# Optimization experiments

Hardware: AMD Instinct MI355X
Metric: run time of the kernel (lower is better)

The kernel has to match this reference:

```python
import jax, jax.numpy as jnp
import numpy as np

N_QUBITS = 12
LAYERS = 8
N_CLASS = 10
BATCH = 2048
FEAT = 3072  # CIFAR-10 flattened 3*32*32
DIM = 2 ** N_QUBITS


def _apply_ry_layer(psi, angles):
    """Apply Ry(angles[q]) to qubit q for all q. psi: [B, 2,...,2] complex.
    kron order in the torch code makes qubit 0 the MSB -> tensor axis q+1."""
    c, s = jnp.cos(angles), jnp.sin(angles)
    for q in range(N_QUBITS):
        rot = jnp.stack([jnp.stack([c[q], -s[q]]), jnp.stack([s[q], c[q]])]).astype(psi.dtype)
        # contract qubit axis with rot (rows index output): psi'[..a..] = rot[a,b] psi[..b..]
        psi = jnp.moveaxis(jnp.tensordot(psi, rot, axes=([q + 1], [1])), -1, q + 1)
    return psi


def _cnot(psi, control, target):
    """CNOT == proj0(c) x I(t) + proj1(c) x X(t): flip target bit where control bit is 1."""
    ca, ta = control + 1, target + 1
    flipped = jnp.flip(psi, axis=ta)          # X on target qubit
    p0 = jax.lax.index_in_dim(psi, 0, axis=ca, keepdims=True)      # control = 0: identity
    p1 = jax.lax.index_in_dim(flipped, 1, axis=ca, keepdims=True)  # control = 1: X
    return jnp.concatenate([p0, p1], axis=ca)


def setup_inputs() -> dict:
    key = jax.random.key(0)
    kx, ka, kw = jax.random.split(key, 3)
    x = jax.random.normal(kx, (BATCH, FEAT), dtype=jnp.float32)
    angles = jax.random.uniform(ka, (LAYERS, N_QUBITS), minval=-0.01, maxval=0.01, dtype=jnp.float32)
    W = jax.random.normal(kw, (N_CLASS, DIM), dtype=jnp.float32) * np.float32(1.0 / np.sqrt(DIM))
    b = jnp.zeros((N_CLASS,), dtype=jnp.float32)
    return {"x": x, "angles": angles, "W": W, "b": b}


def reference(x, angles, W, b):
    B = x.shape[0]
    # CIFAR branch: right-pad features to 2^n, flatten (no-op for 2D), L2-normalize rows
    x = jnp.pad(x, ((0, 0), (0, DIM - x.shape[1])))
    x = x / jnp.linalg.norm(x, axis=1, keepdims=True)
    psi = x.astype(jnp.complex64).reshape((B,) + (2,) * N_QUBITS)
    for l in range(LAYERS):
        psi = _apply_ry_layer(psi, angles[l])
        # cx_linear_layer: CNOT(n-2,n-1), then CNOT(i,i+1) for i = n-3..0
        psi = _cnot(psi, N_QUBITS - 2, N_QUBITS - 1)
        for i in range(N_QUBITS - 3, -1, -1):
            psi = _cnot(psi, i, i + 1)
    probs = (psi.real ** 2 + psi.imag ** 2).reshape(B, DIM)  # Re(conj(psi)*psi)
    return probs @ W.T + b
```

## Files before the change

### kernel.cpp

```cpp
#include <hip/hip_runtime.h>
#include <math.h>

#define LAYERS  8
#define FEAT    3072
#define NCLASS  10
#define DIM     4096
#define ST      68

typedef float v2f __attribute__((ext_vector_type(2)));
typedef float v4f __attribute__((ext_vector_type(4)));

__device__ __forceinline__ int px6c(int r) {
    int u = r ^ (r >> 1); u ^= u >> 2; u ^= u >> 4; return u & 63;
}
__device__ __forceinline__ int gray6(int r) { return (r ^ (r >> 1)) & 63; }

__device__ __forceinline__ float getc(const v2f v[32], int u) {
    return (u & 1) ? v[u >> 1].y : v[u >> 1].x;
}
__device__ __forceinline__ void setc(v2f v[32], int u, float x) {
    if (u & 1) v[u >> 1].y = x; else v[u >> 1].x = x;
}
__device__ __forceinline__ float bpermf(int addr, float x) {
    return __int_as_float(__builtin_amdgcn_ds_bpermute(addr, __float_as_int(x)));
}


__device__ __forceinline__ void butterflies6t(v2f v[32],
                                              const float* __restrict__ tl,
                                              int off) {
    {
        const float tt = tl[off];
#pragma unroll
        for (int i = 0; i < 32; ++i) {
            v2f a = v[i];
            v[i].x = fmaf(-tt, a.y, a.x);
            v[i].y = fmaf( tt, a.x, a.y);
        }
    }
#pragma unroll
    for (int p = 1; p < 6; ++p) {
        const float tt = tl[off - p];
#pragma unroll
        for (int i0 = 0; i0 < 32; ++i0) {
            if (i0 & (1 << (p - 1))) continue;
            const int i1 = i0 | (1 << (p - 1));
            v2f a = v[i0], e = v[i1];
            v[i0].x = fmaf(-tt, e.x, a.x);
            v[i0].y = fmaf(-tt, e.y, a.y);
            v[i1].x = fmaf( tt, a.x, e.x);
            v[i1].y = fmaf( tt, a.y, e.y);
        }
    }
}

__device__ __forceinline__ void butterflies6_renamed_t(v2f v[32],
                                                       const float* __restrict__ tl,
                                                       float psgn) {
    {
        const float tt = tl[11];
#pragma unroll
        for (int k = 0; k < 32; ++k) {
            v2f a = v[k];
            const float te = (k & 1) ? -tt : tt;
            v[k].x = fmaf(-te, a.y, a.x);
            v[k].y = fmaf( te, a.x, a.y);
        }
    }
#pragma unroll
    for (int b = 1; b < 5; ++b) {
        const float tt = tl[11 - b];
#pragma unroll
        for (int m = 0; m < 32; ++m) {
            if (m & (1 << (b - 1))) continue;
            const int part = m ^ ((1 << b) - 1);
            const float tg = (m & (1 << b)) ? -tt : tt;
            v2f A = v[m], E = v[part];
            v[m].x    = fmaf(-tg, E.y, A.x);
            v[m].y    = fmaf(-tg, E.x, A.y);
            v[part].x = fmaf( tg, A.y, E.x);
            v[part].y = fmaf( tg, A.x, E.y);
        }
    }
    {
        const float tt = psgn * tl[6];
#pragma unroll
        for (int m = 0; m < 16; ++m) {
            const int part = m ^ 31;
            v2f A = v[m], E = v[part];
            v[m].x    = fmaf(-tt, E.y, A.x);
            v[m].y    = fmaf(-tt, E.x, A.y);
            v[part].x = fmaf( tt, A.y, E.x);
            v[part].y = fmaf( tt, A.x, E.y);
        }
    }
}

__global__ __launch_bounds__(64)
void qnn_kernel(const float* __restrict__ x,
                const float* __restrict__ ang,
                const float* __restrict__ W,
                const float* __restrict__ bias,
                float* __restrict__ out)
{
    __shared__ __attribute__((aligned(16))) float lds[ST * 64];
    __shared__ float tnt[96];

    const int t = threadIdx.x;
    const int b = blockIdx.x;

    float cprod2;
    {
        float a0 = ang[t];
        float c0 = cosf(a0), s0 = sinf(a0);
        tnt[t] = s0 / c0;
        float pc = c0;
        if (t < 32) {
            float a1 = ang[64 + t];
            float c1 = cosf(a1), s1 = sinf(a1);
            tnt[64 + t] = s1 / c1;
            pc *= c1;
        }
#pragma unroll
        for (int o = 1; o < 64; o <<= 1) pc *= __shfl_xor(pc, o, 64);
        cprod2 = pc * pc;
    }

    v2f v[32];
    {
        const float* xb = x + (size_t)b * FEAT;
#pragma unroll
        for (int r = 0; r < 64; ++r) {
            if (r < FEAT / 64) setc(v, r, xb[64 * r + t]);
            else               setc(v, r, 0.f);
        }
    }

    float invn2;
    {
        v2f s2 = {0.f, 0.f};
#pragma unroll
        for (int i = 0; i < 32; ++i) s2 += v[i] * v[i];
        float ss = s2.x + s2.y;
#pragma unroll
        for (int o = 1; o < 64; o <<= 1) ss += __shfl_xor(ss, o, 64);
        invn2 = cprod2 / ss;
    }

    {
        const int slot = __builtin_amdgcn_s_getreg(4 | (0 << 6) | (3 << 11)) & 7;
#pragma unroll 1
        for (int i = 0; i < slot; ++i) __builtin_amdgcn_s_sleep(12);
    }

    int px = t ^ (t >> 1); px ^= px >> 2; px ^= px >> 4; px &= 63;
    const int A0 = 4 * px;
    const int A1 = 4 * (px ^ 63);
    const int u0 = t & 1;
    const float psgn = u0 ? -1.f : 1.f;
    const int gtl = gray6(t);
    const int bp  = gtl + 32 * ST * u0;
    const int bm  = gtl - 32 * ST * u0;

    {
        const float* tl = tnt;
        butterflies6t(v, tl, 5);
#pragma unroll
        for (int i = 0; i < 16; ++i) {
            v4f q = {v[2 * i].x, v[2 * i].y, v[2 * i + 1].x, v[2 * i + 1].y};
            *(v4f*)(lds + ST * t + 4 * i) = q;
        }
#pragma unroll
        for (int u = 0; u < 64; ++u)
            setc(v, u, lds[t + ST * u]);
        butterflies6t(v, tl, 11);
    }

#pragma unroll 1
    for (int p = 0; p < 4; ++p) {
        {
            const float* tl = tnt + (2 * p + 1) * 12;

            butterflies6_renamed_t(v, tl, psgn);

#pragma unroll
            for (int s = 0; s < 64; ++s) {
                const int g = gray6(s);
                lds[((g & 32) ? bm : bp) + ST * g] = getc(v, s);
            }
#pragma unroll
            for (int i = 0; i < 16; ++i) {
                v4f q = *(const v4f*)(lds + ST * t + 4 * i);
                v[2 * i]     = (v2f){q.x, q.y};
                v[2 * i + 1] = (v2f){q.z, q.w};
            }

            butterflies6t(v, tl, 5);

            if (p < 3) {
                float n[64];
#pragma unroll
                for (int r = 0; r < 64; ++r) {
                    const int srcr = px6c(r);
                    n[r] = bpermf((srcr & 1) ? A1 : A0, getc(v, srcr));
                }
#pragma unroll
                for (int r = 0; r < 64; ++r)
                    setc(v, r, n[r]);
            }
        }

        if (p == 3) break;

        {
            const float* tl = tnt + (2 * p + 2) * 12;

            butterflies6t(v, tl, 5);
#pragma unroll
            for (int i = 0; i < 16; ++i) {
                v4f q = {v[2 * i].x, v[2 * i].y, v[2 * i + 1].x, v[2 * i + 1].y};
                *(v4f*)(lds + ST * t + 4 * i) = q;
            }
#pragma unroll
            for (int u = 0; u < 64; ++u)
                setc(v, u, lds[t + ST * u]);
            butterflies6t(v, tl, 11);
        }
    }

#pragma unroll
    for (int i = 0; i < 32; ++i) {
        const int g0 = 64 * gray6(2 * i);
        const int g1 = 64 * (gray6(2 * i) ^ 1);
        lds[g0 + gtl]        = v[i].x * v[i].x;
        lds[g1 + (gtl ^ 32)] = v[i].y * v[i].y;
    }

    float acc[NCLASS];
#pragma unroll
    for (int c = 0; c < NCLASS; ++c) acc[c] = 0.f;

#pragma unroll 1
    for (int k = 0; k < 16; ++k) {
        const v4f q4 = *(const v4f*)(lds + 4 * t + 256 * k);
        const float* wp = W + 4 * t + 256 * k;
#pragma unroll
        for (int c = 0; c < NCLASS; ++c) {
            const v4f w4 = *(const v4f*)(wp + c * DIM);
            acc[c] += q4.x * w4.x + q4.y * w4.y + q4.z * w4.z + q4.w * w4.w;
        }
    }

#pragma unroll
    for (int c = 0; c < NCLASS; ++c) {
        float a = acc[c];
#pragma unroll
        for (int o = 1; o < 64; o <<= 1) a += __shfl_xor(a, o, 64);
        if (t == 0) out[b * NCLASS + c] = fmaf(a, invn2, bias[c]);
    }
}

extern "C" void kernel_launch(void* const* d_in, const int* in_sizes, int n_in,
                              void* d_out, int out_size, void* d_ws, size_t ws_size,
                              hipStream_t stream) {
    const float* x    = (const float*)d_in[0];
    const float* ang  = (const float*)d_in[1];
    const float* W    = (const float*)d_in[2];
    const float* bias = (const float*)d_in[3];
    float* out = (float*)d_out;
    const int batch = in_sizes[0] / FEAT;
    qnn_kernel<<<batch, 64, 0, stream>>>(x, ang, W, bias, out);
}
```

Before: 108.2 us.

## Replace LDS transposes with cross-lane DPP/swizzle/permlane butterfly stages

```diff
diff --git a/kernel.cpp b/kernel.cpp
--- a/kernel.cpp
+++ b/kernel.cpp
@@ -5,10 +5,10 @@
 #define FEAT    3072
 #define NCLASS  10
 #define DIM     4096
-#define ST      68
 
 typedef float v2f __attribute__((ext_vector_type(2)));
 typedef float v4f __attribute__((ext_vector_type(4)));
+typedef unsigned u32x2 __attribute__((ext_vector_type(2)));
 
 __device__ __forceinline__ int px6c(int r) {
     int u = r ^ (r >> 1); u ^= u >> 2; u ^= u >> 4; return u & 63;
@@ -54,47 +54,64 @@
     }
 }
 
-__device__ __forceinline__ void butterflies6_renamed_t(v2f v[32],
-                                                       const float* __restrict__ tl,
-                                                       float psgn) {
-    {
-        const float tt = tl[11];
-#pragma unroll
-        for (int k = 0; k < 32; ++k) {
-            v2f a = v[k];
-            const float te = (k & 1) ? -tt : tt;
-            v[k].x = fmaf(-te, a.y, a.x);
-            v[k].y = fmaf( te, a.x, a.y);
-        }
-    }
-#pragma unroll
-    for (int b = 1; b < 5; ++b) {
-        const float tt = tl[11 - b];
-#pragma unroll
-        for (int m = 0; m < 32; ++m) {
-            if (m & (1 << (b - 1))) continue;
-            const int part = m ^ ((1 << b) - 1);
-            const float tg = (m & (1 << b)) ? -tt : tt;
-            v2f A = v[m], E = v[part];
-            v[m].x    = fmaf(-tg, E.y, A.x);
-            v[m].y    = fmaf(-tg, E.x, A.y);
-            v[part].x = fmaf( tg, A.y, E.x);
-            v[part].y = fmaf( tg, A.x, E.y);
-        }
-    }
-    {
-        const float tt = psgn * tl[6];
-#pragma unroll
-        for (int m = 0; m < 16; ++m) {
-            const int part = m ^ 31;
-            v2f A = v[m], E = v[part];
-            v[m].x    = fmaf(-tt, E.y, A.x);
-            v[m].y    = fmaf(-tt, E.x, A.y);
-            v[part].x = fmaf( tt, A.y, E.x);
-            v[part].y = fmaf( tt, A.x, E.y);
-        }
-    }
-}
+template<int CTRL>
+__device__ __forceinline__ void laneStageDpp(v2f v[32], float ts) {
+#pragma unroll
+    for (int i = 0; i < 32; ++i) {
+        float ax = __int_as_float(__builtin_amdgcn_update_dpp(
+            0, __float_as_int(v[i].x), CTRL, 0xF, 0xF, true));
+        float ay = __int_as_float(__builtin_amdgcn_update_dpp(
+            0, __float_as_int(v[i].y), CTRL, 0xF, 0xF, true));
+        v[i].x = fmaf(ts, ax, v[i].x);
+        v[i].y = fmaf(ts, ay, v[i].y);
+    }
+}
+
+template<int IMM>
+__device__ __forceinline__ void laneStageSwz(v2f v[32], float ts) {
+#pragma unroll
+    for (int i = 0; i < 32; ++i) {
+        float ax = __int_as_float(__builtin_amdgcn_ds_swizzle(__float_as_int(v[i].x), IMM));
+        float ay = __int_as_float(__builtin_amdgcn_ds_swizzle(__float_as_int(v[i].y), IMM));
+        v[i].x = fmaf(ts, ax, v[i].x);
+        v[i].y = fmaf(ts, ay, v[i].y);
+    }
+}
+
+__device__ __forceinline__ void laneStagePl32(v2f v[32], float tt) {
+#pragma unroll
+    for (int i = 0; i < 32; ++i) {
+        u32x2 r = __builtin_amdgcn_permlane32_swap(
+            __float_as_int(v[i].x), __float_as_int(v[i].y), false, false);
+        float lo = __int_as_float(r.x), hi = __int_as_float(r.y);
+        float nlo = fmaf(-tt, hi, lo);
+        float nhi = fmaf( tt, lo, hi);
+        u32x2 r2 = __builtin_amdgcn_permlane32_swap(
+            __float_as_int(nlo), __float_as_int(nhi), false, false);
+        v[i].x = __int_as_float(r2.x);
+        v[i].y = __int_as_float(r2.y);
+    }
+}
+
+#if __has_builtin(__builtin_amdgcn_permlane16_swap)
+#define HAVE_PL16 1
+__device__ __forceinline__ void laneStagePl16(v2f v[32], float tt) {
+#pragma unroll
+    for (int i = 0; i < 32; ++i) {
+        u32x2 r = __builtin_amdgcn_permlane16_swap(
+            __float_as_int(v[i].x), __float_as_int(v[i].y), false, false);
+        float lo = __int_as_float(r.x), hi = __int_as_float(r.y);
+        float nlo = fmaf(-tt, hi, lo);
+        float nhi = fmaf( tt, lo, hi);
+        u32x2 r2 = __builtin_amdgcn_permlane16_swap(
+            __float_as_int(nlo), __float_as_int(nhi), false, false);
+        v[i].x = __int_as_float(r2.x);
+        v[i].y = __int_as_float(r2.y);
+    }
+}
+#else
+#define HAVE_PL16 0
+#endif
 
 __global__ __launch_bounds__(64)
 void qnn_kernel(const float* __restrict__ x,
@@ -103,7 +120,7 @@
                 const float* __restrict__ bias,
                 float* __restrict__ out)
 {
-    __shared__ __attribute__((aligned(16))) float lds[ST * 64];
+    __shared__ __attribute__((aligned(16))) float lds[DIM];
     __shared__ float tnt[96];
 
     const int t = threadIdx.x;
@@ -156,75 +173,54 @@
     int px = t ^ (t >> 1); px ^= px >> 2; px ^= px >> 4; px &= 63;
     const int A0 = 4 * px;
     const int A1 = 4 * (px ^ 63);
-    const int u0 = t & 1;
-    const float psgn = u0 ? -1.f : 1.f;
     const int gtl = gray6(t);
-    const int bp  = gtl + 32 * ST * u0;
-    const int bm  = gtl - 32 * ST * u0;
-
-    {
-        const float* tl = tnt;
-        butterflies6t(v, tl, 5);
-#pragma unroll
-        for (int i = 0; i < 16; ++i) {
-            v4f q = {v[2 * i].x, v[2 * i].y, v[2 * i + 1].x, v[2 * i + 1].y};
-            *(v4f*)(lds + ST * t + 4 * i) = q;
-        }
-#pragma unroll
-        for (int u = 0; u < 64; ++u)
-            setc(v, u, lds[t + ST * u]);
-        butterflies6t(v, tl, 11);
-    }
+    const int NEGBIT = (int)0x80000000u;
+    const int sm0 = (t & 1)  ? 0 : NEGBIT;
+    const int sm1 = (t & 2)  ? 0 : NEGBIT;
+    const int sm2 = (t & 4)  ? 0 : NEGBIT;
+    const int sm3 = (t & 8)  ? 0 : NEGBIT;
+#if !HAVE_PL16
+    const int sm4 = (t & 16) ? 0 : NEGBIT;
+    const int a16 = 4 * (t ^ 16);
+#endif
 
 #pragma unroll 1
-    for (int p = 0; p < 4; ++p) {
+    for (int p = 0; p < LAYERS; ++p) {
+        float tb[12];
+#pragma unroll
+        for (int q = 0; q < 12; ++q) tb[q] = tnt[12 * p + q];
+
+        laneStageSwz<0x101F>(v, __int_as_float(__float_as_int(tb[9]) ^ sm2));
+        laneStageDpp<0xB1>  (v, __int_as_float(__float_as_int(tb[11]) ^ sm0));
+        laneStageSwz<0x201F>(v, __int_as_float(__float_as_int(tb[8]) ^ sm3));
+        laneStageDpp<0x4E>  (v, __int_as_float(__float_as_int(tb[10]) ^ sm1));
+#if HAVE_PL16
+        laneStagePl16(v, tb[7]);
+#else
         {
-            const float* tl = tnt + (2 * p + 1) * 12;
-
-            butterflies6_renamed_t(v, tl, psgn);
-
-#pragma unroll
-            for (int s = 0; s < 64; ++s) {
-                const int g = gray6(s);
-                lds[((g & 32) ? bm : bp) + ST * g] = getc(v, s);
+            const float ts = __int_as_float(__float_as_int(tb[7]) ^ sm4);
+#pragma unroll
+            for (int i = 0; i < 32; ++i) {
+                float ax = bpermf(a16, v[i].x);
+                float ay = bpermf(a16, v[i].y);
+                v[i].x = fmaf(ts, ax, v[i].x);
+                v[i].y = fmaf(ts, ay, v[i].y);
             }
-#pragma unroll
-            for (int i = 0; i < 16; ++i) {
-                v4f q = *(const v4f*)(lds + ST * t + 4 * i);
-                v[2 * i]     = (v2f){q.x, q.y};
-                v[2 * i + 1] = (v2f){q.z, q.w};
+        }
+#endif
+        laneStagePl32(v, tb[6]);
+        butterflies6t(v, tb, 5);
+
+        if (p < LAYERS - 1) {
+            float n[64];
+#pragma unroll
+            for (int r = 0; r < 64; ++r) {
+                const int srcr = px6c(r);
+                n[r] = bpermf((srcr & 1) ? A1 : A0, getc(v, srcr));
             }
-
-            butterflies6t(v, tl, 5);
-
-            if (p < 3) {
-                float n[64];
-#pragma unroll
-                for (int r = 0; r < 64; ++r) {
-                    const int srcr = px6c(r);
-                    n[r] = bpermf((srcr & 1) ? A1 : A0, getc(v, srcr));
-                }
-#pragma unroll
-                for (int r = 0; r < 64; ++r)
-                    setc(v, r, n[r]);
-            }
-        }
-
-        if (p == 3) break;
-
-        {
-            const float* tl = tnt + (2 * p + 2) * 12;
-
-            butterflies6t(v, tl, 5);
-#pragma unroll
-            for (int i = 0; i < 16; ++i) {
-                v4f q = {v[2 * i].x, v[2 * i].y, v[2 * i + 1].x, v[2 * i + 1].y};
-                *(v4f*)(lds + ST * t + 4 * i) = q;
-            }
-#pragma unroll
-            for (int u = 0; u < 64; ++u)
-                setc(v, u, lds[t + ST * u]);
-            butterflies6t(v, tl, 11);
+#pragma unroll
+            for (int r = 0; r < 64; ++r)
+                setc(v, r, n[r]);
         }
     }
 
```

Result: slower. 120.8 us (+11.6%).
